# Performance work log

Measured on AMD Instinct MI355X. Metric: run time of the kernel, lower is better.

## Reference

```python
import jax, jax.numpy as jnp
import numpy as np

B, L = 16, 2048
D_IN, D_MODEL, N_STATE = 64, 256, 64
N_LAYERS = 4
D_MID1, D_MID2, D_OUT = 128, 64, 32


def _layernorm(x, g, b):
    # x: (B, L, H), normalize over H (biased variance, eps=1e-5 like torch)
    mu = x.mean(-1, keepdims=True)
    var = x.var(-1, keepdims=True)
    return (x - mu) / jnp.sqrt(var + 1e-5) * g + b


def setup_inputs() -> dict:
    key = jax.random.key(0)
    ks = jax.random.split(key, 16)
    H, Nh = D_MODEL, N_STATE // 2
    x = jax.random.normal(ks[0], (B, L, D_IN), jnp.float32)
    enc_w = jax.random.normal(ks[1], (D_IN, H), jnp.float32) / np.sqrt(D_IN).astype(np.float32)
    enc_b = jnp.zeros((H,), jnp.float32)
    # S4D kernel params (per layer): dt ~ loguniform[1e-3, 1e-1]
    log_dt = jax.random.uniform(ks[2], (N_LAYERS, H), jnp.float32) * (np.log(0.1) - np.log(0.001)) + np.log(0.001)
    log_dt = log_dt.astype(jnp.float32)
    C_re = jax.random.normal(ks[3], (N_LAYERS, H, Nh), jnp.float32)
    C_im = jax.random.normal(ks[4], (N_LAYERS, H, Nh), jnp.float32)
    log_A_real = jnp.log(0.5 * jnp.ones((N_LAYERS, H, Nh), jnp.float32))
    A_imag = jnp.broadcast_to(np.pi * jnp.arange(Nh, dtype=jnp.float32), (N_LAYERS, H, Nh)).copy()
    D_skip = jax.random.normal(ks[5], (N_LAYERS, H), jnp.float32)
    # output_linear: Conv1d(H, 2H, kernel_size=1) + GLU
    w_out = jax.random.normal(ks[6], (N_LAYERS, 2 * H, H), jnp.float32) / np.sqrt(H).astype(np.float32)
    b_out = jnp.zeros((N_LAYERS, 2 * H), jnp.float32)
    ln_g = jnp.ones((N_LAYERS, H), jnp.float32)
    ln_b = jnp.zeros((N_LAYERS, H), jnp.float32)
    dec_w1 = jax.random.normal(ks[7], (H, D_MID1), jnp.float32) / np.sqrt(H).astype(np.float32)
    dec_b1 = jnp.zeros((D_MID1,), jnp.float32)
    dec_w2 = jax.random.normal(ks[8], (D_MID1, D_MID2), jnp.float32) / np.sqrt(D_MID1).astype(np.float32)
    dec_b2 = jnp.zeros((D_MID2,), jnp.float32)
    dec_w3 = jax.random.normal(ks[9], (D_MID2, D_OUT), jnp.float32) / np.sqrt(D_MID2).astype(np.float32)
    dec_b3 = jnp.zeros((D_OUT,), jnp.float32)
    return dict(x=x, enc_w=enc_w, enc_b=enc_b, log_dt=log_dt, C_re=C_re, C_im=C_im,
                log_A_real=log_A_real, A_imag=A_imag, D_skip=D_skip, w_out=w_out, b_out=b_out,
                ln_g=ln_g, ln_b=ln_b, dec_w1=dec_w1, dec_b1=dec_b1, dec_w2=dec_w2, dec_b2=dec_b2,
                dec_w3=dec_w3, dec_b3=dec_b3)


def reference(x, enc_w, enc_b, log_dt, C_re, C_im, log_A_real, A_imag, D_skip,
              w_out, b_out, ln_g, ln_b, dec_w1, dec_b1, dec_w2, dec_b2, dec_w3, dec_b3):
    h = x @ enc_w + enc_b            # (B, L, H)
    h = jnp.swapaxes(h, -1, -2)      # (B, H, L) -- transposed S4D
    Ls = h.shape[-1]
    t = jnp.arange(Ls, dtype=jnp.float32)
    for i in range(N_LAYERS):
        # --- S4D kernel via Vandermonde over discretized diagonal A ---
        dt = jnp.exp(log_dt[i])                       # (H,)
        A = -jnp.exp(log_A_real[i]) + 1j * A_imag[i]  # (H, N/2)
        C = C_re[i] + 1j * C_im[i]                    # (H, N/2)
        dtA = A * dt[:, None]
        Ck = C * (jnp.exp(dtA) - 1.0) / A
        K = 2.0 * jnp.einsum('hn,hnl->hl', Ck, jnp.exp(dtA[:, :, None] * t)).real  # (H, L)
        # --- FFT convolution (linear conv via 2L padding) + skip ---
        y = jnp.fft.irfft(jnp.fft.rfft(h, n=2 * Ls) * jnp.fft.rfft(K, n=2 * Ls), n=2 * Ls)[..., :Ls]
        y = y + h * D_skip[i][:, None]
        y = jax.nn.gelu(y, approximate=False)
        # output_linear: 1x1 conv to 2H then GLU over channel dim
        y = jnp.einsum('oh,bhl->bol', w_out[i], y) + b_out[i][:, None]
        a, g = jnp.split(y, 2, axis=1)
        z = a * jax.nn.sigmoid(g)
        # residual + post-LayerNorm (prenorm=False)
        h = z + h
        h = jnp.swapaxes(_layernorm(jnp.swapaxes(h, -1, -2), ln_g[i], ln_b[i]), -1, -2)
    pooled = jnp.swapaxes(h, -1, -2).mean(-2)  # (B, H)
    o = jax.nn.relu(pooled @ dec_w1 + dec_b1)
    o = jax.nn.relu(o @ dec_w2 + dec_b2)
    return o @ dec_w3 + dec_b3
```

## Files before the change

kernel.cpp:

```cpp
#include <hip/hip_runtime.h>

#define B_SZ 16
#define L_SZ 2048
#define DIN 64
#define H_SZ 256
#define NH 32
#define NL 4
#define TC 64
#define NTC 32
#define YROW (H_SZ + 8)

typedef __attribute__((ext_vector_type(8))) __bf16 bf16x8;
typedef __attribute__((ext_vector_type(4))) float f32x4;

__device__ __forceinline__ unsigned short f2b(float f) {
  unsigned int u = __builtin_bit_cast(unsigned int, f);
  unsigned int r = u + 0x7fffu + ((u >> 16) & 1u);
  return (unsigned short)(r >> 16);
}
__device__ __forceinline__ float b2f(unsigned short u) {
  unsigned int v = ((unsigned int)u) << 16;
  return __builtin_bit_cast(float, v);
}
__device__ __forceinline__ float gelu_exact(float v) {
  return 0.5f * v * (1.f + erff(v * 0.70710678118654752f));
}
__device__ __forceinline__ int yswz(int row, int col) {
  return (row * YROW + col) ^ (((row >> 3) & 7) << 3);
}

__launch_bounds__(512, 4)
__global__ void k_encoder(const float* __restrict__ x, const float* __restrict__ w,
                          const float* __restrict__ bias, float* __restrict__ hbuf) {
  __shared__ __align__(16) unsigned short Wh[128][72];
  __shared__ __align__(16) unsigned short Wl[128][72];
  __shared__ __align__(16) unsigned short xh[128][72];
  __shared__ __align__(16) unsigned short xl[128][72];
  int tid = threadIdx.x;
  int blk = blockIdx.x;
  int b = blk >> 5;
  int lt = (blk >> 1) & 15;
  int hh = blk & 1;

#pragma unroll
  for (int i = 0; i < 16; ++i) {
    int flat = i * 512 + tid;
    int d = flat >> 7, hl = flat & 127;
    float v = w[d * H_SZ + (hh << 7) + hl];
    unsigned short hv = f2b(v);
    Wh[hl][d] = hv; Wl[hl][d] = f2b(v - b2f(hv));
  }
  {
    int l = tid >> 2, d0 = (tid & 3) << 4;
    const float* src = x + ((size_t)(b * L_SZ + (lt << 7) + l) << 6) + d0;
    unsigned short* dh = &xh[l][d0];
    unsigned short* dl = &xl[l][d0];
#pragma unroll
    for (int jj = 0; jj < 4; ++jj) {
      float4 v = *(const float4*)(src + jj * 4);
      unsigned short h0 = f2b(v.x); dh[jj * 4 + 0] = h0; dl[jj * 4 + 0] = f2b(v.x - b2f(h0));
      unsigned short h1 = f2b(v.y); dh[jj * 4 + 1] = h1; dl[jj * 4 + 1] = f2b(v.y - b2f(h1));
      unsigned short h2 = f2b(v.z); dh[jj * 4 + 2] = h2; dl[jj * 4 + 2] = f2b(v.z - b2f(h2));
      unsigned short h3 = f2b(v.w); dh[jj * 4 + 3] = h3; dl[jj * 4 + 3] = f2b(v.w - b2f(h3));
    }
  }
  __syncthreads();

  int wv = tid >> 6, lane = tid & 63;
  int lrow = lane & 15, lk8 = (lane >> 4) << 3;
  int rsub = (lane >> 4) << 2;
  f32x4 acc[8];
#pragma unroll
  for (int ct = 0; ct < 8; ++ct) acc[ct] = (f32x4){0.f, 0.f, 0.f, 0.f};
#pragma unroll
  for (int kk = 0; kk < 2; ++kk) {
    bf16x8 ah = *(const bf16x8*)&Wh[(wv << 4) + lrow][(kk << 5) + lk8];
    bf16x8 al = *(const bf16x8*)&Wl[(wv << 4) + lrow][(kk << 5) + lk8];
#pragma unroll
    for (int ct = 0; ct < 8; ++ct) {
      bf16x8 bh = *(const bf16x8*)&xh[(ct << 4) + lrow][(kk << 5) + lk8];
      bf16x8 bl = *(const bf16x8*)&xl[(ct << 4) + lrow][(kk << 5) + lk8];
      acc[ct] = __builtin_amdgcn_mfma_f32_16x16x32_bf16(ah, bh, acc[ct], 0, 0, 0);
      acc[ct] = __builtin_amdgcn_mfma_f32_16x16x32_bf16(ah, bl, acc[ct], 0, 0, 0);
      acc[ct] = __builtin_amdgcn_mfma_f32_16x16x32_bf16(al, bh, acc[ct], 0, 0, 0);
    }
  }
  float bi[4];
#pragma unroll
  for (int r = 0; r < 4; ++r) bi[r] = bias[(hh << 7) + (wv << 4) + rsub + r];
#pragma unroll
  for (int ct = 0; ct < 8; ++ct) {
    int lglob = (lt << 7) + (ct << 4) + lrow;
#pragma unroll
    for (int r = 0; r < 4; ++r) {
      int hglob = (hh << 7) + (wv << 4) + rsub + r;
      hbuf[((size_t)(b * H_SZ + hglob) << 11) + lglob] = acc[ct][r] + bi[r];
    }
  }
}

__global__ void k_cvtw(const float* __restrict__ w, unsigned short* __restrict__ wbf, int n) {
  int i = blockIdx.x * 256 + threadIdx.x;
  if (i < n) wbf[i] = f2b(w[i]);
}

__global__ void k_params(const float* __restrict__ log_dt, const float* __restrict__ log_A_real,
                         const float* __restrict__ A_imag, const float* __restrict__ C_re,
                         const float* __restrict__ C_im, float* __restrict__ par) {
  int id = blockIdx.x * 256 + threadIdx.x;
  if (id >= NL * H_SZ * NH) return;
  int i = id >> 13;
  int hn = id & 8191;
  int h = hn >> 5;
  float dt = expf(log_dt[i * H_SZ + h]);
  float Ar = -expf(log_A_real[(size_t)i * H_SZ * NH + hn]);
  float Ai = A_imag[(size_t)i * H_SZ * NH + hn];
  float dr = dt * Ar, di = dt * Ai;
  float e = expf(dr), sn, cs;
  sincosf(di, &sn, &cs);
  float lr = e * cs, li = e * sn;
  float eT = expf((float)TC * dr), snT, csT;
  sincosf((float)TC * di, &snT, &csT);
  float Cr = C_re[(size_t)i * H_SZ * NH + hn], Ci = C_im[(size_t)i * H_SZ * NH + hn];
  float wr = lr - 1.f, wi = li;
  float pr = Cr * wr - Ci * wi;
  float pi = Cr * wi + Ci * wr;
  float inv = 2.f / fmaf(Ar, Ar, Ai * Ai);
  float4* p = (float4*)(par + (size_t)id * 8);
  p[0] = make_float4(lr, li, (pr * Ar + pi * Ai) * inv, (pi * Ar - pr * Ai) * inv);
  p[1] = make_float4(eT * csT, eT * snT, 0.f, 0.f);
}

__launch_bounds__(512, 1)
__global__ void k_ssm(const float* __restrict__ hbuf, float2* __restrict__ sF2,
                      const float* __restrict__ par, const float* __restrict__ D_skip,
                      unsigned short* __restrict__ yloc) {
  __shared__ __align__(16) unsigned short xbh[256][72];
  __shared__ __align__(16) unsigned short xbl[256][72];
  __shared__ __align__(16) unsigned short Uh[64][72];
  __shared__ __align__(16) unsigned short Ul[64][72];
  __shared__ __align__(16) unsigned short Th[64][72];
  __shared__ __align__(16) unsigned short Tl[64][72];
  __shared__ __align__(16) unsigned short Wh[64][72];
  __shared__ __align__(16) unsigned short Wl[64][72];
  __shared__ float Kc[64];
  int tid = threadIdx.x;
  int h = blockIdx.x;
  float* Wm = (float*)&xbh[0][0];

  if (tid < 64) {
    int n = tid >> 1, q = tid & 1;
    const float* pb = par + (size_t)(h * NH + n) * 8;
    float lr = pb[0], li = pb[1], c2r = pb[2], c2i = pb[3];
    float pr = lr, pi = li;
    if (q) {
      float sr = lr, si = li;
#pragma unroll
      for (int t = 0; t < 5; ++t) { float nr2 = sr * sr - si * si; si = 2.f * sr * si; sr = nr2; }
      pr = sr * lr - si * li; pi = sr * li + si * lr;
    }
    int p = q << 5;
    for (int s = 0; s < 32; ++s, ++p) {
      Wm[p * 66 + 2 * n] = c2r * pr - c2i * pi;
      Wm[p * 66 + 2 * n + 1] = -(c2r * pi + c2i * pr);
      float nr2 = pr * lr - pi * li;
      pi = pr * li + pi * lr;
      pr = nr2;
    }
  }
  __syncthreads();
  if (tid < 64) {
    float kv = 0.f;
    if (tid == 0) {
      for (int n = 0; n < 32; ++n) kv += par[(size_t)(h * NH + n) * 8 + 2];
    } else {
      for (int n = 0; n < 32; ++n) kv += Wm[(tid - 1) * 66 + 2 * n];
    }
    Kc[tid] = kv;
  }
  {
    int base = tid * 8;
    int row = base >> 6, col0 = base & 63;
#pragma unroll
    for (int e = 0; e < 8; ++e) {
      float v = Wm[row * 66 + col0 + e];
      unsigned short hv = f2b(v);
      Wh[row][col0 + e] = hv; Wl[row][col0 + e] = f2b(v - b2f(hv));
    }
  }
  __syncthreads();
  {
    int base = tid * 8;
    int row = base >> 6, col0 = base & 63;
#pragma unroll
    for (int e = 0; e < 8; ++e) {
      int col = col0 + e;
      float v = (col <= row) ? Kc[row - col] : 0.f;
      unsigned short hv = f2b(v);
      Th[row][col] = hv; Tl[row][col] = f2b(v - b2f(hv));
    }
  }
  if (tid < 64) {
    int n = tid >> 1, q = tid & 1;
    const float* pb = par + (size_t)(h * NH + n) * 8;
    float lr = pb[0], li = pb[1];
    float pr = 1.f, pi = 0.f;
    if (q) {
      float sr = lr, si = li;
#pragma unroll
      for (int t = 0; t < 5; ++t) { float nr2 = sr * sr - si * si; si = 2.f * sr * si; sr = nr2; }
      pr = sr; pi = si;
    }
    int p = q << 5;
    for (int s = 0; s < 32; ++s, ++p) {
      int col = 63 - p;
      unsigned short hr = f2b(pr);
      Uh[2 * n][col] = hr; Ul[2 * n][col] = f2b(pr - b2f(hr));
      unsigned short hm = f2b(pi);
      Uh[2 * n + 1][col] = hm; Ul[2 * n + 1][col] = f2b(pi - b2f(hm));
      float nr2 = pr * lr - pi * li;
      pi = pr * li + pi * lr;
      pr = nr2;
    }
  }

  int wv = tid >> 6, lane = tid & 63;
  int lrow = lane & 15, lk8 = (lane >> 4) << 3;
  int rt = wv >> 1;
  int ct0 = (wv & 1) << 3;
  int rsub = (lane >> 4) << 2;
  float Dh = D_skip[h];

  for (int half = 0; half < 2; ++half) {
    __syncthreads();
    {
      int colh = tid >> 1, j0 = (tid & 1) << 5;
      int b = (half << 3) + (colh >> 5), c = colh & 31;
      const float* src = hbuf + ((size_t)(b * H_SZ + h) << 11) + (c << 6) + j0;
      unsigned short* dh = &xbh[colh][j0];
      unsigned short* dl = &xbl[colh][j0];
#pragma unroll
      for (int jj = 0; jj < 8; ++jj) {
        float4 v = *(const float4*)(src + jj * 4);
        unsigned short h0 = f2b(v.x); dh[jj * 4 + 0] = h0; dl[jj * 4 + 0] = f2b(v.x - b2f(h0));
        unsigned short h1 = f2b(v.y); dh[jj * 4 + 1] = h1; dl[jj * 4 + 1] = f2b(v.y - b2f(h1));
        unsigned short h2 = f2b(v.z); dh[jj * 4 + 2] = h2; dl[jj * 4 + 2] = f2b(v.z - b2f(h2));
        unsigned short h3 = f2b(v.w); dh[jj * 4 + 3] = h3; dl[jj * 4 + 3] = f2b(v.w - b2f(h3));
      }
    }
    __syncthreads();
    {
      f32x4 uacc[8];
#pragma unroll
      for (int ct = 0; ct < 8; ++ct) uacc[ct] = (f32x4){0.f, 0.f, 0.f, 0.f};
#pragma unroll
      for (int kk = 0; kk < 2; ++kk) {
        bf16x8 ah = *(const bf16x8*)&Uh[(rt << 4) + lrow][(kk << 5) + lk8];
        bf16x8 al = *(const bf16x8*)&Ul[(rt << 4) + lrow][(kk << 5) + lk8];
#pragma unroll
        for (int ct = 0; ct < 8; ++ct) {
          int col = ((ct0 + ct) << 4) + lrow;
          bf16x8 bh = *(const bf16x8*)&xbh[col][(kk << 5) + lk8];
          bf16x8 bl = *(const bf16x8*)&xbl[col][(kk << 5) + lk8];
          uacc[ct] = __builtin_amdgcn_mfma_f32_16x16x32_bf16(ah, bh, uacc[ct], 0, 0, 0);
          uacc[ct] = __builtin_amdgcn_mfma_f32_16x16x32_bf16(ah, bl, uacc[ct], 0, 0, 0);
          uacc[ct] = __builtin_amdgcn_mfma_f32_16x16x32_bf16(al, bh, uacc[ct], 0, 0, 0);
        }
      }
      int n0 = (rt << 3) + ((lane >> 4) << 1);
#pragma unroll
      for (int ct = 0; ct < 8; ++ct) {
        int colg = (half << 8) + ((ct0 + ct) << 4) + lrow;
        float2* o = sF2 + (size_t)colg * (H_SZ * NH) + h * NH + n0;
        o[0] = make_float2(uacc[ct][0], uacc[ct][1]);
        o[1] = make_float2(uacc[ct][2], uacc[ct][3]);
      }
    }
    f32x4 acc[8];
#pragma unroll
    for (int ct = 0; ct < 8; ++ct) acc[ct] = (f32x4){0.f, 0.f, 0.f, 0.f};
#pragma unroll
    for (int kk = 0; kk < 2; ++kk) {
      bf16x8 ah = *(const bf16x8*)&Th[(rt << 4) + lrow][(kk << 5) + lk8];
      bf16x8 al = *(const bf16x8*)&Tl[(rt << 4) + lrow][(kk << 5) + lk8];
#pragma unroll
      for (int ct = 0; ct < 8; ++ct) {
        int col = ((ct0 + ct) << 4) + lrow;
        bf16x8 bh = *(const bf16x8*)&xbh[col][(kk << 5) + lk8];
        bf16x8 bl = *(const bf16x8*)&xbl[col][(kk << 5) + lk8];
        acc[ct] = __builtin_amdgcn_mfma_f32_16x16x32_bf16(ah, bh, acc[ct], 0, 0, 0);
        acc[ct] = __builtin_amdgcn_mfma_f32_16x16x32_bf16(ah, bl, acc[ct], 0, 0, 0);
        acc[ct] = __builtin_amdgcn_mfma_f32_16x16x32_bf16(al, bh, acc[ct], 0, 0, 0);
      }
    }
    {
#pragma unroll
      for (int ct = 0; ct < 8; ++ct) {
        int col = ((ct0 + ct) << 4) + lrow;
        int row = (rt << 4) + rsub;
        ushort4 xh4 = *(const ushort4*)&xbh[col][row];
        ushort4 xl4 = *(const ushort4*)&xbl[col][row];
        acc[ct][0] = fmaf(Dh, b2f(xh4.x) + b2f(xl4.x), acc[ct][0]);
        acc[ct][1] = fmaf(Dh, b2f(xh4.y) + b2f(xl4.y), acc[ct][1]);
        acc[ct][2] = fmaf(Dh, b2f(xh4.z) + b2f(xl4.z), acc[ct][2]);
        acc[ct][3] = fmaf(Dh, b2f(xh4.w) + b2f(xl4.w), acc[ct][3]);
      }
    }
    __syncthreads();
    if (tid < 256) {
      int b = (half << 3) + (tid >> 5), n = tid & 31;
      const float* pb = par + (size_t)(h * NH + n) * 8;
      float lTr = pb[4], lTi = pb[5];
      float cr = 0.f, ci = 0.f;
      float2* p0 = sF2 + (size_t)(b << 5) * (H_SZ * NH) + h * NH + n;
      const size_t cstride = H_SZ * NH;
      float2 f = p0[0];
      for (int c = 0; c < NTC; ++c) {
        float2 fn = f;
        if (c + 1 < NTC) fn = p0[(size_t)(c + 1) * cstride];
        p0[(size_t)c * cstride] = make_float2(cr, ci);
        float nr = fmaf(lTr, cr, f.x); nr = fmaf(-lTi, ci, nr);
        float ni = fmaf(lTr, ci, f.y); ni = fmaf(lTi, cr, ni);
        cr = nr; ci = ni;
        f = fn;
      }
    }
    __syncthreads();
    {
      int colh = tid >> 1, n0 = (tid & 1) << 4;
      int colg = (half << 8) + colh;
      const float2* cp = sF2 + (size_t)colg * (H_SZ * NH) + h * NH;
#pragma unroll
      for (int n = 0; n < 16; ++n) {
        float2 s = cp[n0 + n];
        int k2 = 2 * (n0 + n);
        unsigned short hr = f2b(s.x);
        xbh[colh][k2] = hr; xbl[colh][k2] = f2b(s.x - b2f(hr));
        unsigned short hm = f2b(s.y);
        xbh[colh][k2 + 1] = hm; xbl[colh][k2 + 1] = f2b(s.y - b2f(hm));
      }
    }
    __syncthreads();
#pragma unroll
    for (int kk = 0; kk < 2; ++kk) {
      bf16x8 ah = *(const bf16x8*)&Wh[(rt << 4) + lrow][(kk << 5) + lk8];
      bf16x8 al = *(const bf16x8*)&Wl[(rt << 4) + lrow][(kk << 5) + lk8];
#pragma unroll
      for (int ct = 0; ct < 8; ++ct) {
        int col = ((ct0 + ct) << 4) + lrow;
        bf16x8 bh = *(const bf16x8*)&xbh[col][(kk << 5) + lk8];
        bf16x8 bl = *(const bf16x8*)&xbl[col][(kk << 5) + lk8];
        acc[ct] = __builtin_amdgcn_mfma_f32_16x16x32_bf16(ah, bh, acc[ct], 0, 0, 0);
        acc[ct] = __builtin_amdgcn_mfma_f32_16x16x32_bf16(ah, bl, acc[ct], 0, 0, 0);
        acc[ct] = __builtin_amdgcn_mfma_f32_16x16x32_bf16(al, bh, acc[ct], 0, 0, 0);
      }
    }
#pragma unroll
    for (int ct = 0; ct < 8; ++ct) {
      int colg = (half << 8) + ((ct0 + ct) << 4) + lrow;
      ushort4 o;
      o.x = f2b(gelu_exact(acc[ct][0]));
      o.y = f2b(gelu_exact(acc[ct][1]));
      o.z = f2b(gelu_exact(acc[ct][2]));
      o.w = f2b(gelu_exact(acc[ct][3]));
      *(ushort4*)(yloc + (size_t)h * (B_SZ * L_SZ) + (size_t)colg * 64 + (rt << 4) + rsub) = o;
    }
  }
}

__launch_bounds__(1024, 4)
__global__ void k_layer2(float* __restrict__ hbuf, const unsigned short* __restrict__ yloc,
                         const unsigned short* __restrict__ wbf,
                         const float* __restrict__ b_out,
                         const float* __restrict__ ln_g, const float* __restrict__ ln_b,
                         float* __restrict__ pooledPart, int last) {
  __shared__ __align__(16) unsigned short yt[TC * YROW];
  __shared__ float part[TC][16][2];
  __shared__ float stats[TC][2];
  int tid = threadIdx.x;
  int b = blockIdx.x >> 5;
  int c = blockIdx.x & 31;
  int l0 = c << 6;

  {
    int h = tid >> 2, q = tid & 3;
    const unsigned short* yp2 = yloc + (size_t)h * (B_SZ * L_SZ) + b * L_SZ + l0 + (q << 4);
#pragma unroll
    for (int jj = 0; jj < 16; jj += 4) {
      ushort4 yv = *(const ushort4*)(yp2 + jj);
      int jb = (q << 4) + jj;
      yt[yswz(jb + 0, h)] = yv.x;
      yt[yswz(jb + 1, h)] = yv.y;
      yt[yswz(jb + 2, h)] = yv.z;
      yt[yswz(jb + 3, h)] = yv.w;
    }
  }
  __syncthreads();
  {
    int w = tid >> 6, lane = tid & 63;
    int lrow = lane & 15, lk8 = (lane >> 4) << 3;
    f32x4 accA[4], accG[4];
    f32x4 zed = {0.f, 0.f, 0.f, 0.f};
#pragma unroll
    for (int jt = 0; jt < 4; ++jt) { accA[jt] = zed; accG[jt] = zed; }
    const unsigned short* wA = wbf + ((w << 4) + lrow) * H_SZ;
    const unsigned short* wG = wA + 256 * H_SZ;
#pragma unroll
    for (int k0 = 0; k0 < H_SZ; k0 += 32) {
      bf16x8 a0 = *(const bf16x8*)(wA + k0 + lk8);
      bf16x8 a1 = *(const bf16x8*)(wG + k0 + lk8);
#pragma unroll
      for (int jt = 0; jt < 4; ++jt) {
        bf16x8 bb = *(const bf16x8*)&yt[yswz((jt << 4) + lrow, k0 + lk8)];
        accA[jt] = __builtin_amdgcn_mfma_f32_16x16x32_bf16(a0, bb, accA[jt], 0, 0, 0);
        accG[jt] = __builtin_amdgcn_mfma_f32_16x16x32_bf16(a1, bb, accG[jt], 0, 0, 0);
      }
    }
    __syncthreads();
    int rbase = (lane >> 4) << 2;
    float bA[4], bG[4];
#pragma unroll
    for (int r = 0; r < 4; ++r) {
      bA[r] = b_out[(w << 4) + rbase + r];
      bG[r] = b_out[256 + (w << 4) + rbase + r];
    }
#pragma unroll
    for (int jt = 0; jt < 4; ++jt) {
      ushort4 o;
      float a0 = accA[jt][0] + bA[0], g0 = accG[jt][0] + bG[0];
      float a1 = accA[jt][1] + bA[1], g1 = accG[jt][1] + bG[1];
      float a2 = accA[jt][2] + bA[2], g2 = accG[jt][2] + bG[2];
      float a3 = accA[jt][3] + bA[3], g3 = accG[jt][3] + bG[3];
      o.x = f2b(a0 / (1.f + expf(-g0)));
      o.y = f2b(a1 / (1.f + expf(-g1)));
      o.z = f2b(a2 / (1.f + expf(-g2)));
      o.w = f2b(a3 / (1.f + expf(-g3)));
      *(ushort4*)&yt[yswz((jt << 4) + lrow, (w << 4) + rbase)] = o;
    }
  }
  __syncthreads();
  int j = tid & 63, hg = tid >> 6;
  float vreg[16];
  {
    const float* xc = hbuf + (b * H_SZ + (hg << 4)) * L_SZ + l0 + j;
    float s = 0.f, sq = 0.f;
    ushort4 za = *(const ushort4*)&yt[yswz(j, (hg << 4) + 0)];
    ushort4 zb = *(const ushort4*)&yt[yswz(j, (hg << 4) + 4)];
    ushort4 zc = *(const ushort4*)&yt[yswz(j, (hg << 4) + 8)];
    ushort4 zd = *(const ushort4*)&yt[yswz(j, (hg << 4) + 12)];
    unsigned short zz[16] = {za.x, za.y, za.z, za.w, zb.x, zb.y, zb.z, zb.w,
                             zc.x, zc.y, zc.z, zc.w, zd.x, zd.y, zd.z, zd.w};
#pragma unroll
    for (int k = 0; k < 16; ++k) {
      float v = b2f(zz[k]) + xc[(size_t)k * L_SZ];
      vreg[k] = v;
      s += v; sq = fmaf(v, v, sq);
    }
    part[j][hg][0] = s; part[j][hg][1] = sq;
  }
  __syncthreads();
  if (tid < TC) {
    float s = 0.f, sq = 0.f;
#pragma unroll
    for (int g = 0; g < 16; ++g) { s += part[tid][g][0]; sq += part[tid][g][1]; }
    float mu = s * (1.f / 256.f);
    float var = sq * (1.f / 256.f) - mu * mu;
    stats[tid][0] = mu;
    stats[tid][1] = rsqrtf(var + 1e-5f);
  }
  __syncthreads();
  {
    float mu = stats[j][0], rs = stats[j][1];
    if (!last) {
      float* xo = hbuf + (b * H_SZ + (hg << 4)) * L_SZ + l0 + j;
#pragma unroll
      for (int k = 0; k < 16; ++k) {
        int hh = (hg << 4) + k;
        xo[(size_t)k * L_SZ] = (vreg[k] - mu) * rs * ln_g[hh] + ln_b[hh];
      }
    } else {
#pragma unroll
      for (int k = 0; k < 16; ++k) {
        int hh = (hg << 4) + k;
        yt[yswz(j, hh)] = f2b((vreg[k] - mu) * rs * ln_g[hh] + ln_b[hh]);
      }
      __syncthreads();
      if (tid < H_SZ) {
        float s = 0.f;
        for (int jj = 0; jj < TC; ++jj) s += b2f(yt[yswz(jj, tid)]);
        pooledPart[(((b << 5) + c) << 8) + tid] = s;
      }
    }
  }
}

__global__ void k_pool(const float* __restrict__ pooledPart, float* __restrict__ P) {
  int b = blockIdx.x, hh = threadIdx.x;
  float s = 0.f;
#pragma unroll
  for (int cpart = 0; cpart < 32; ++cpart)
    s += pooledPart[(((b << 5) + cpart) << 8) + hh];
  P[(b << 8) + hh] = s * (1.f / 2048.f);
}

__global__ void k_dec(const float* __restrict__ P,
                      const float* __restrict__ w1, const float* __restrict__ b1,
                      const float* __restrict__ w2, const float* __restrict__ b2,
                      const float* __restrict__ w3, const float* __restrict__ b3,
                      float* __restrict__ out) {
  __shared__ float Pr[256];
  __shared__ float O1[128];
  __shared__ float O2[64];
  int b = blockIdx.x, tid = threadIdx.x;
  Pr[tid] = P[(b << 8) + tid];
  __syncthreads();
  if (tid < 128) {
    float acc = b1[tid];
    for (int d = 0; d < 256; ++d) acc = fmaf(Pr[d], w1[(d << 7) + tid], acc);
    O1[tid] = fmaxf(acc, 0.f);
  }
  __syncthreads();
  if (tid < 64) {
    float acc = b2[tid];
    for (int d = 0; d < 128; ++d) acc = fmaf(O1[d], w2[(d << 6) + tid], acc);
    O2[tid] = fmaxf(acc, 0.f);
  }
  __syncthreads();
  if (tid < 32) {
    float acc = b3[tid];
    for (int d = 0; d < 64; ++d) acc = fmaf(O2[d], w3[(d << 5) + tid], acc);
    out[(b << 5) + tid] = acc;
  }
}

extern "C" void kernel_launch(void* const* d_in, const int* in_sizes, int n_in,
                              void* d_out, int out_size, void* d_ws, size_t ws_size,
                              hipStream_t stream) {
  const float* x          = (const float*)d_in[0];
  const float* enc_w      = (const float*)d_in[1];
  const float* enc_b      = (const float*)d_in[2];
  const float* log_dt     = (const float*)d_in[3];
  const float* C_re       = (const float*)d_in[4];
  const float* C_im       = (const float*)d_in[5];
  const float* log_A_real = (const float*)d_in[6];
  const float* A_imag     = (const float*)d_in[7];
  const float* D_skip     = (const float*)d_in[8];
  const float* w_out      = (const float*)d_in[9];
  const float* b_out      = (const float*)d_in[10];
  const float* ln_g       = (const float*)d_in[11];
  const float* ln_b       = (const float*)d_in[12];
  const float* dw1        = (const float*)d_in[13];
  const float* db1        = (const float*)d_in[14];
  const float* dw2        = (const float*)d_in[15];
  const float* db2        = (const float*)d_in[16];
  const float* dw3        = (const float*)d_in[17];
  const float* db3        = (const float*)d_in[18];

  char* ws = (char*)d_ws;
  float* hbuf = (float*)ws;
  float2* sF2 = (float2*)(ws + 33554432);
  unsigned short* yloc = (unsigned short*)(ws + 67108864);
  unsigned short* wbf = (unsigned short*)(ws + 83886080);
  float* par = (float*)(ws + 84934656);
  float* pooledPart = (float*)(ws + 85983232);
  float* P = (float*)(ws + 86507520);

  k_encoder<<<512, 512, 0, stream>>>(x, enc_w, enc_b, hbuf);
  k_cvtw<<<2048, 256, 0, stream>>>(w_out, wbf, NL * 512 * H_SZ);
  k_params<<<128, 256, 0, stream>>>(log_dt, log_A_real, A_imag, C_re, C_im, par);
  const size_t PAR_STRIDE = (size_t)H_SZ * NH * 8;
  for (int i = 0; i < NL; ++i) {
    const float* pari = par + i * PAR_STRIDE;
    k_ssm<<<256, 512, 0, stream>>>(hbuf, sF2, pari, D_skip + i * H_SZ, yloc);
    k_layer2<<<512, 1024, 0, stream>>>(hbuf, yloc,
                                       wbf + i * 512 * H_SZ, b_out + i * 512,
                                       ln_g + i * H_SZ, ln_b + i * H_SZ,
                                       pooledPart, (i == NL - 1) ? 1 : 0);
  }
  k_pool<<<16, 256, 0, stream>>>(pooledPart, P);
  k_dec<<<16, 256, 0, stream>>>(P, dw1, db1, dw2, db2, dw3, db3, (float*)d_out);
}
```

Baseline: 371.8 us.

## Keep chunk-state scan in shared memory instead of global sF2 scratch

The per-chunk state contributions (uacc) were written to a large global scratch buffer, scanned across chunks there, and read back into shared memory. Now they are split into bf16 hi/lo pairs and written directly into the shared xbh/xbl tiles, and the sequential chunk scan reads and writes those tiles in place. This removes a global round trip of about 32 MB per layer and one reload pass. In exchange, uacc registers stay live across the T-matmul, and the scan now does bf16 splitting and merging on its inputs.

```diff
diff --git a/kernel.cpp b/kernel.cpp
--- a/kernel.cpp
+++ b/kernel.cpp
@@ -132,9 +132,8 @@
 }
 
 __launch_bounds__(512, 1)
-__global__ void k_ssm(const float* __restrict__ hbuf, float2* __restrict__ sF2,
-                      const float* __restrict__ par, const float* __restrict__ D_skip,
-                      unsigned short* __restrict__ yloc) {
+__global__ void k_ssm(const float* __restrict__ hbuf, const float* __restrict__ par,
+                      const float* __restrict__ D_skip, unsigned short* __restrict__ yloc) {
   __shared__ __align__(16) unsigned short xbh[256][72];
   __shared__ __align__(16) unsigned short xbl[256][72];
   __shared__ __align__(16) unsigned short Uh[64][72];
@@ -249,31 +248,21 @@
       }
     }
     __syncthreads();
-    {
-      f32x4 uacc[8];
-#pragma unroll
-      for (int ct = 0; ct < 8; ++ct) uacc[ct] = (f32x4){0.f, 0.f, 0.f, 0.f};
-#pragma unroll
-      for (int kk = 0; kk < 2; ++kk) {
-        bf16x8 ah = *(const bf16x8*)&Uh[(rt << 4) + lrow][(kk << 5) + lk8];
-        bf16x8 al = *(const bf16x8*)&Ul[(rt << 4) + lrow][(kk << 5) + lk8];
-#pragma unroll
-        for (int ct = 0; ct < 8; ++ct) {
-          int col = ((ct0 + ct) << 4) + lrow;
-          bf16x8 bh = *(const bf16x8*)&xbh[col][(kk << 5) + lk8];
-          bf16x8 bl = *(const bf16x8*)&xbl[col][(kk << 5) + lk8];
-          uacc[ct] = __builtin_amdgcn_mfma_f32_16x16x32_bf16(ah, bh, uacc[ct], 0, 0, 0);
-          uacc[ct] = __builtin_amdgcn_mfma_f32_16x16x32_bf16(ah, bl, uacc[ct], 0, 0, 0);
-          uacc[ct] = __builtin_amdgcn_mfma_f32_16x16x32_bf16(al, bh, uacc[ct], 0, 0, 0);
-        }
-      }
-      int n0 = (rt << 3) + ((lane >> 4) << 1);
+    f32x4 uacc[8];
+#pragma unroll
+    for (int ct = 0; ct < 8; ++ct) uacc[ct] = (f32x4){0.f, 0.f, 0.f, 0.f};
+#pragma unroll
+    for (int kk = 0; kk < 2; ++kk) {
+      bf16x8 ah = *(const bf16x8*)&Uh[(rt << 4) + lrow][(kk << 5) + lk8];
+      bf16x8 al = *(const bf16x8*)&Ul[(rt << 4) + lrow][(kk << 5) + lk8];
 #pragma unroll
       for (int ct = 0; ct < 8; ++ct) {
-        int colg = (half << 8) + ((ct0 + ct) << 4) + lrow;
-        float2* o = sF2 + (size_t)colg * (H_SZ * NH) + h * NH + n0;
-        o[0] = make_float2(uacc[ct][0], uacc[ct][1]);
-        o[1] = make_float2(uacc[ct][2], uacc[ct][3]);
+        int col = ((ct0 + ct) << 4) + lrow;
+        bf16x8 bh = *(const bf16x8*)&xbh[col][(kk << 5) + lk8];
+        bf16x8 bl = *(const bf16x8*)&xbl[col][(kk << 5) + lk8];
+        uacc[ct] = __builtin_amdgcn_mfma_f32_16x16x32_bf16(ah, bh, uacc[ct], 0, 0, 0);
+        uacc[ct] = __builtin_amdgcn_mfma_f32_16x16x32_bf16(ah, bl, uacc[ct], 0, 0, 0);
+        uacc[ct] = __builtin_amdgcn_mfma_f32_16x16x32_bf16(al, bh, uacc[ct], 0, 0, 0);
       }
     }
     f32x4 acc[8];
@@ -307,37 +296,37 @@
       }
     }
     __syncthreads();
+    {
+      int n0 = (rt << 3) + ((lane >> 4) << 1);
+#pragma unroll
+      for (int ct = 0; ct < 8; ++ct) {
+        int colh = ((ct0 + ct) << 4) + lrow;
+        ushort4 oh, ol;
+        oh.x = f2b(uacc[ct][0]); ol.x = f2b(uacc[ct][0] - b2f(oh.x));
+        oh.y = f2b(uacc[ct][1]); ol.y = f2b(uacc[ct][1] - b2f(oh.y));
+        oh.z = f2b(uacc[ct][2]); ol.z = f2b(uacc[ct][2] - b2f(oh.z));
+        oh.w = f2b(uacc[ct][3]); ol.w = f2b(uacc[ct][3] - b2f(oh.w));
+        *(ushort4*)&xbh[colh][2 * n0] = oh;
+        *(ushort4*)&xbl[colh][2 * n0] = ol;
+      }
+    }
+    __syncthreads();
     if (tid < 256) {
-      int b = (half << 3) + (tid >> 5), n = tid & 31;
+      int bb = tid >> 5, n = tid & 31;
       const float* pb = par + (size_t)(h * NH + n) * 8;
       float lTr = pb[4], lTi = pb[5];
       float cr = 0.f, ci = 0.f;
-      float2* p0 = sF2 + (size_t)(b << 5) * (H_SZ * NH) + h * NH + n;
-      const size_t cstride = H_SZ * NH;
-      float2 f = p0[0];
       for (int c = 0; c < NTC; ++c) {
-        float2 fn = f;
-        if (c + 1 < NTC) fn = p0[(size_t)(c + 1) * cstride];
-        p0[(size_t)c * cstride] = make_float2(cr, ci);
-        float nr = fmaf(lTr, cr, f.x); nr = fmaf(-lTi, ci, nr);
-        float ni = fmaf(lTr, ci, f.y); ni = fmaf(lTi, cr, ni);
+        int col = (bb << 5) + c;
+        float fr = b2f(xbh[col][2 * n]) + b2f(xbl[col][2 * n]);
+        float fi = b2f(xbh[col][2 * n + 1]) + b2f(xbl[col][2 * n + 1]);
+        unsigned short hr = f2b(cr);
+        xbh[col][2 * n] = hr; xbl[col][2 * n] = f2b(cr - b2f(hr));
+        unsigned short hm = f2b(ci);
+        xbh[col][2 * n + 1] = hm; xbl[col][2 * n + 1] = f2b(ci - b2f(hm));
+        float nr = fmaf(lTr, cr, fr); nr = fmaf(-lTi, ci, nr);
+        float ni = fmaf(lTr, ci, fi); ni = fmaf(lTi, cr, ni);
         cr = nr; ci = ni;
-        f = fn;
-      }
-    }
-    __syncthreads();
-    {
-      int colh = tid >> 1, n0 = (tid & 1) << 4;
-      int colg = (half << 8) + colh;
-      const float2* cp = sF2 + (size_t)colg * (H_SZ * NH) + h * NH;
-#pragma unroll
-      for (int n = 0; n < 16; ++n) {
-        float2 s = cp[n0 + n];
-        int k2 = 2 * (n0 + n);
-        unsigned short hr = f2b(s.x);
-        xbh[colh][k2] = hr; xbl[colh][k2] = f2b(s.x - b2f(hr));
-        unsigned short hm = f2b(s.y);
-        xbh[colh][k2 + 1] = hm; xbl[colh][k2 + 1] = f2b(s.y - b2f(hm));
       }
     }
     __syncthreads();
@@ -558,12 +547,11 @@
 
   char* ws = (char*)d_ws;
   float* hbuf = (float*)ws;
-  float2* sF2 = (float2*)(ws + 33554432);
-  unsigned short* yloc = (unsigned short*)(ws + 67108864);
-  unsigned short* wbf = (unsigned short*)(ws + 83886080);
-  float* par = (float*)(ws + 84934656);
-  float* pooledPart = (float*)(ws + 85983232);
-  float* P = (float*)(ws + 86507520);
+  unsigned short* yloc = (unsigned short*)(ws + 33554432);
+  unsigned short* wbf = (unsigned short*)(ws + 50331648);
+  float* par = (float*)(ws + 51380224);
+  float* pooledPart = (float*)(ws + 52428800);
+  float* P = (float*)(ws + 52953088);
 
   k_encoder<<<512, 512, 0, stream>>>(x, enc_w, enc_b, hbuf);
   k_cvtw<<<2048, 256, 0, stream>>>(w_out, wbf, NL * 512 * H_SZ);
@@ -571,7 +559,7 @@
   const size_t PAR_STRIDE = (size_t)H_SZ * NH * 8;
   for (int i = 0; i < NL; ++i) {
     const float* pari = par + i * PAR_STRIDE;
-    k_ssm<<<256, 512, 0, stream>>>(hbuf, sF2, pari, D_skip + i * H_SZ, yloc);
+    k_ssm<<<256, 512, 0, stream>>>(hbuf, pari, D_skip + i * H_SZ, yloc);
     k_layer2<<<512, 1024, 0, stream>>>(hbuf, yloc,
                                        wbf + i * 512 * H_SZ, b_out + i * 512,
                                        ln_g + i * H_SZ, ln_b + i * H_SZ,
```

After: 321.2 us. 1.16x faster.
